# Kernel tuning notes

Measured on AMD Instinct MI355X. Metric: run time of the kernel, lower is better.

Reference implementation:

```python
import jax, jax.numpy as jnp
import numpy as np

HEAD_DIM = 32
NUM_HEADS = 8
NUM_ACTIONS = 16
IN_FEATURES = 512
HIDDEN = NUM_HEADS * HEAD_DIM
EPS = 1e-6


def _l2norm(v):
    return v / jnp.sqrt(jnp.sum(v * v, axis=-1, keepdims=True) + EPS)


def setup_inputs() -> dict:
    key = jax.random.key(0)
    ks = jax.random.split(key, 12)
    B, S = 4, 2048
    sc_x = 1.0 / np.sqrt(IN_FEATURES)
    sc_a = 1.0 / np.sqrt(NUM_ACTIONS)
    sc_h = 1.0 / np.sqrt(HIDDEN)
    return {
        "x": jax.random.normal(ks[0], (B, S, IN_FEATURES), jnp.float32),
        "action": jax.random.normal(ks[1], (B, S, NUM_ACTIONS), jnp.float32),
        "mask": jnp.zeros((B, S), jnp.float32),
        "carry": jnp.zeros((B, NUM_HEADS, HEAD_DIM, HEAD_DIM), jnp.float32),
        "Wq": jax.random.normal(ks[2], (IN_FEATURES, HIDDEN), jnp.float32) * sc_x,
        "Wk": jax.random.normal(ks[3], (IN_FEATURES, HIDDEN), jnp.float32) * sc_x,
        "Wv": jax.random.normal(ks[4], (IN_FEATURES, HIDDEN), jnp.float32) * sc_x,
        "Wbeta": jax.random.normal(ks[5], (IN_FEATURES, NUM_HEADS), jnp.float32) * sc_x,
        "Walpha": jax.random.normal(ks[6], (IN_FEATURES, NUM_HEADS), jnp.float32) * sc_x,
        "Wku": jax.random.normal(ks[7], (NUM_ACTIONS, HIDDEN), jnp.float32) * sc_a,
        "Wvu": jax.random.normal(ks[8], (NUM_ACTIONS, HIDDEN), jnp.float32) * sc_a,
        "Wgamma": jax.random.normal(ks[9], (NUM_ACTIONS, NUM_HEADS), jnp.float32) * sc_a,
        "rms_scale": jnp.ones((HIDDEN,), jnp.float32),
        "Wout": jax.random.normal(ks[10], (HIDDEN, IN_FEATURES), jnp.float32) * sc_h,
        "bout": jnp.zeros((IN_FEATURES,), jnp.float32),
    }


def reference(x, action, mask, carry, Wq, Wk, Wv, Wbeta, Walpha, Wku, Wvu,
              Wgamma, rms_scale, Wout, bout):
    B, S, F = x.shape
    H, D = NUM_HEADS, HEAD_DIM

    q_s = jax.nn.silu((x @ Wq).reshape(B, S, H, D))
    k_s = jax.nn.silu((x @ Wk).reshape(B, S, H, D))
    v_s = (x @ Wv).reshape(B, S, H, D)
    beta = jax.nn.sigmoid(x @ Wbeta)            # (B,S,H)
    A = jax.nn.sigmoid(x @ Walpha)              # (B,S,H)
    k_u = jax.nn.silu((action @ Wku).reshape(B, S, H, D))
    v_u = (action @ Wvu).reshape(B, S, H, D)
    Bg = jax.nn.sigmoid(action @ Wgamma)        # (B,S,H)

    q_s = _l2norm(q_s)
    k_s = _l2norm(k_s)
    k_u = _l2norm(k_u)

    eye = jnp.eye(D, dtype=x.dtype)
    kkT = jnp.einsum('bshi,bshj->bshij', k_s, k_s)
    delta = eye - beta[..., None, None] * kkT                      # (B,S,H,D,D)
    decay = A[..., None, None] * delta * (1.0 - mask[:, :, None, None, None])
    drift = Bg[..., None, None] * jnp.einsum('bshi,bshj->bshij', v_u, k_u)
    write = beta[..., None, None] * jnp.einsum('bshi,bshj->bshij', v_s, k_s)
    update = jnp.matmul(drift, delta) + write

    def binop(lhs, rhs):
        a_i, b_i = lhs
        a_j, b_j = rhs
        return (jnp.matmul(a_i, a_j), jnp.matmul(b_i, a_j) + b_j)

    cum_decay, hidden = jax.lax.associative_scan(binop, (decay, update), axis=1)
    hidden = jnp.matmul(carry[:, None], cum_decay) + hidden        # (B,S,H,D,D)

    out = jnp.einsum('bshij,bshj->bshi', hidden, q_s).reshape(B, S, H * D)
    out = out * jax.lax.rsqrt(jnp.mean(out * out, axis=-1, keepdims=True) + EPS)
    out = out * rms_scale
    y = out @ Wout + bout
    new_carry = hidden[:, -1]
    return (new_carry, y)
```

## Files before the change

kernel.cpp:

```cpp
#include <hip/hip_runtime.h>
#include <math.h>

constexpr int B_    = 4;
constexpr int S_    = 2048;
constexpr int F_    = 512;
constexpr int H_    = 8;
constexpr int D_    = 32;
constexpr int HID_  = 256;
constexpr int NA_   = 16;
constexpr int ROWS_ = B_ * S_;
constexpr int CHUNK_= 32;
constexpr int NC_   = S_ / CHUNK_;
constexpr int T_    = 16;
constexpr int NT_   = CHUNK_ / T_;
constexpr int BH_   = B_ * H_;

typedef __attribute__((ext_vector_type(8))) short short8;
typedef __attribute__((ext_vector_type(4))) float f32x4;
typedef unsigned short u16;

__device__ __forceinline__ float sigmoidf_(float x) { return 1.0f / (1.0f + expf(-x)); }

__device__ __forceinline__ u16 f2bf(float f) {
    unsigned u = __float_as_uint(f);
    return (u16)((u + 0x7FFF + ((u >> 16) & 1)) >> 16);
}
__device__ __forceinline__ float bf2f(u16 h) {
    return __uint_as_float(((unsigned)h) << 16);
}
__device__ __forceinline__ void bfsplit(float x, u16& hi, u16& lo) {
    hi = f2bf(x);
    lo = f2bf(x - bf2f(hi));
}

__device__ __forceinline__ unsigned swz(unsigned r, unsigned cbyte) {
    return cbyte ^ (((r >> 1) & 3) << 4);
}

__global__ __launch_bounds__(256) void conv_x_kernel(
    const float* __restrict__ x, u16* __restrict__ xh, u16* __restrict__ xl)
{
    const int idx = blockIdx.x * 256 + threadIdx.x;
    const float4 v = ((const float4*)x)[idx];
    ushort4 h, l;
    bfsplit(v.x, h.x, l.x); bfsplit(v.y, h.y, l.y);
    bfsplit(v.z, h.z, l.z); bfsplit(v.w, h.w, l.w);
    ((ushort4*)xh)[idx] = h;
    ((ushort4*)xl)[idx] = l;
}

__global__ __launch_bounds__(256) void conv_w_kernel(
    const float* __restrict__ Wq, const float* __restrict__ Wk,
    const float* __restrict__ Wv, const float* __restrict__ Wout,
    u16* __restrict__ wth, u16* __restrict__ wtl,
    u16* __restrict__ woth, u16* __restrict__ wotl)
{
    const int z = blockIdx.z;
    const float* src; u16 *dh, *dl; int R, C;
    if (z < 3) {
        src = (z == 0) ? Wq : (z == 1) ? Wk : Wv;
        R = 512; C = 256;
        dh = wth + (size_t)z * 256 * 512; dl = wtl + (size_t)z * 256 * 512;
    } else {
        src = Wout; R = 256; C = 512; dh = woth; dl = wotl;
    }
    const int r0 = blockIdx.x * 32, c0 = blockIdx.y * 32;
    if (r0 >= R || c0 >= C) return;
    __shared__ float tile[32][33];
    const int tx = threadIdx.x & 31, ty = threadIdx.x >> 5;
    #pragma unroll
    for (int i = 0; i < 4; i++)
        tile[ty + i * 8][tx] = src[(size_t)(r0 + ty + i * 8) * C + c0 + tx];
    __syncthreads();
    #pragma unroll
    for (int i = 0; i < 4; i++) {
        const float v = tile[tx][ty + i * 8];
        const size_t o = (size_t)(c0 + ty + i * 8) * R + r0 + tx;
        u16 h, l; bfsplit(v, h, l);
        dh[o] = h; dl[o] = l;
    }
}

__global__ __launch_bounds__(256) void conv_ba_kernel(
    const float* __restrict__ Wb, const float* __restrict__ Wa,
    u16* __restrict__ wbah, u16* __restrict__ wbal)
{
    const int idx = blockIdx.x * 256 + threadIdx.x;
    const int j = idx >> 9, k = idx & 511;
    const float v = (j < 8) ? Wb[(size_t)k * 8 + j] : Wa[(size_t)k * 8 + (j - 8)];
    u16 h, l; bfsplit(v, h, l);
    wbah[(size_t)j * 512 + k] = h;
    wbal[(size_t)j * 512 + k] = l;
}

__global__ __launch_bounds__(128) void mfma_gemm_kernel(
    const u16* __restrict__ Ah, const u16* __restrict__ Al,
    const u16* __restrict__ Bth, const u16* __restrict__ Btl,
    float* __restrict__ Cbase, int K, int N,
    int btStride, int cStride, const float* __restrict__ bias)
{
    const u16* bh_p = Bth + (size_t)blockIdx.z * btStride;
    const u16* bl_p = Btl + (size_t)blockIdx.z * btStride;
    float* C = Cbase + (size_t)blockIdx.z * cStride;

    __shared__ u16 lAh[128 * 32], lAl[128 * 32];
    __shared__ u16 lBh[64 * 32],  lBl[64 * 32];

    const int t    = threadIdx.x;
    const int wave = t >> 6;
    const int lane = t & 63;
    const int lr   = lane & 15;
    const int lk   = lane >> 4;
    const int row0 = blockIdx.x * 128;
    const int col0 = blockIdx.y * 64;

    f32x4 acc[4][4];
    #pragma unroll
    for (int i = 0; i < 4; i++)
        #pragma unroll
        for (int j = 0; j < 4; j++) acc[i][j] = (f32x4){0.f, 0.f, 0.f, 0.f};

    for (int k0 = 0; k0 < K; k0 += 32) {
        #pragma unroll
        for (int u = 0; u < 4; u++) {
            const int slot = t + u * 128;
            const int r = slot >> 2, cq = slot & 3;
            const size_t g = (size_t)(row0 + r) * K + k0 + cq * 8;
            const unsigned bo = r * 64 + swz(r, cq * 16);
            *(uint4*)((char*)lAh + bo) = *(const uint4*)(Ah + g);
            *(uint4*)((char*)lAl + bo) = *(const uint4*)(Al + g);
        }
        #pragma unroll
        for (int u = 0; u < 2; u++) {
            const int slot = t + u * 128;
            const int r = slot >> 2, cq = slot & 3;
            const size_t g = (size_t)(col0 + r) * K + k0 + cq * 8;
            const unsigned bo = r * 64 + swz(r, cq * 16);
            *(uint4*)((char*)lBh + bo) = *(const uint4*)(bh_p + g);
            *(uint4*)((char*)lBl + bo) = *(const uint4*)(bl_p + g);
        }
        __syncthreads();

        short8 ah[4], al[4];
        #pragma unroll
        for (int tm = 0; tm < 4; tm++) {
            const int r = wave * 64 + tm * 16 + lr;
            const unsigned bo = r * 64 + swz(r, lk * 16);
            ah[tm] = *(const short8*)((const char*)lAh + bo);
            al[tm] = *(const short8*)((const char*)lAl + bo);
        }
        #pragma unroll
        for (int tn = 0; tn < 4; tn++) {
            const int r = tn * 16 + lr;
            const unsigned bo = r * 64 + swz(r, lk * 16);
            const short8 bh = *(const short8*)((const char*)lBh + bo);
            const short8 bl = *(const short8*)((const char*)lBl + bo);
            #pragma unroll
            for (int tm = 0; tm < 4; tm++) {
                acc[tm][tn] = __builtin_amdgcn_mfma_f32_16x16x32_bf16(
                    ah[tm], bh, acc[tm][tn], 0, 0, 0);
                acc[tm][tn] = __builtin_amdgcn_mfma_f32_16x16x32_bf16(
                    ah[tm], bl, acc[tm][tn], 0, 0, 0);
                acc[tm][tn] = __builtin_amdgcn_mfma_f32_16x16x32_bf16(
                    al[tm], bh, acc[tm][tn], 0, 0, 0);
            }
        }
        __syncthreads();
    }

    #pragma unroll
    for (int tm = 0; tm < 4; tm++) {
        #pragma unroll
        for (int tn = 0; tn < 4; tn++) {
            const int col = col0 + tn * 16 + lr;
            const float b = bias ? bias[col] : 0.0f;
            #pragma unroll
            for (int v = 0; v < 4; v++) {
                const int row = row0 + wave * 64 + tm * 16 + lk * 4 + v;
                C[(size_t)row * N + col] = acc[tm][tn][v] + b;
            }
        }
    }
}

__global__ __launch_bounds__(256) void gemm_act_kernel(
    const float* __restrict__ act, const float* __restrict__ Wku,
    const float* __restrict__ Wvu, const float* __restrict__ Wg,
    float* __restrict__ ku, float* __restrict__ vu, float* __restrict__ bg)
{
    const int bid = blockIdx.x;
    if (bid < ROWS_ * 64 / 256) {
        const int idx = bid * 256 + threadIdx.x;
        const int row = idx >> 6, q = idx & 63, col = q * 4;
        float a[16];
        #pragma unroll
        for (int u = 0; u < 4; u++)
            *(float4*)&a[u*4] = *(const float4*)(act + (size_t)row * NA_ + u * 4);
        float4 accK = {0,0,0,0}, accV = {0,0,0,0};
        #pragma unroll
        for (int kk = 0; kk < NA_; kk++) {
            const float4 wk = *(const float4*)(Wku + (size_t)kk * HID_ + col);
            const float4 wv = *(const float4*)(Wvu + (size_t)kk * HID_ + col);
            accK.x += a[kk]*wk.x; accK.y += a[kk]*wk.y; accK.z += a[kk]*wk.z; accK.w += a[kk]*wk.w;
            accV.x += a[kk]*wv.x; accV.y += a[kk]*wv.y; accV.z += a[kk]*wv.z; accV.w += a[kk]*wv.w;
        }
        *(float4*)(ku + (size_t)row * HID_ + col) = accK;
        *(float4*)(vu + (size_t)row * HID_ + col) = accV;
    } else {
        const int idx = (bid - ROWS_ * 64 / 256) * 256 + threadIdx.x;
        const int row = idx >> 3, c = idx & 7;
        const float* a = act + (size_t)row * NA_;
        float acc = 0.0f;
        #pragma unroll
        for (int kk = 0; kk < NA_; kk++) acc += a[kk] * Wg[kk * H_ + c];
        bg[(size_t)row * H_ + c] = sigmoidf_(acc);
    }
}

__global__ __launch_bounds__(256) void silu_norm_kernel(
    float* __restrict__ q, float* __restrict__ k, float* __restrict__ ku)
{
    const int t = threadIdx.x;
    const int d = t & 31;
    const size_t g = (size_t)blockIdx.x * 8 + (t >> 5);
    const size_t idx = g * 32 + d;
    float* bufs[3] = { q, k, ku };
    #pragma unroll
    for (int a = 0; a < 3; a++) {
        float x = bufs[a][idx];
        float v = x * (1.0f / (1.0f + expf(-x)));
        float ss = v * v;
        ss += __shfl_xor(ss, 1);  ss += __shfl_xor(ss, 2);  ss += __shfl_xor(ss, 4);
        ss += __shfl_xor(ss, 8);  ss += __shfl_xor(ss, 16);
        bufs[a][idx] = v * rsqrtf(ss + 1e-6f);
    }
}

__global__ __launch_bounds__(256) void scan_pass1(
    const float* __restrict__ kbuf, const float* __restrict__ vbuf,
    const float* __restrict__ kubuf, const float* __restrict__ vubuf,
    const float* __restrict__ bab, const float* __restrict__ gammab,
    const float* __restrict__ mask,
    float* __restrict__ cumA, float* __restrict__ cumB)
{
    const int bh = blockIdx.x;
    const int c  = blockIdx.y;
    const int b  = bh >> 3, h = bh & 7;
    const int t  = threadIdx.x;
    const int i  = t >> 3;
    const int j0 = (t & 7) * 4;
    __shared__ float lk [T_][32];
    __shared__ float lv [T_][32];
    __shared__ float lku[T_][32];
    __shared__ float lvu[T_][32];
    __shared__ float lsc[T_][4];

    float M[4], Cc[4];
    #pragma unroll
    for (int jj = 0; jj < 4; jj++) { M[jj] = (i == j0 + jj) ? 1.0f : 0.0f; Cc[jj] = 0.0f; }

    const float* g0 = (t < 128) ? kbuf  : vbuf;
    const float* g1 = (t < 128) ? kubuf : vubuf;
    const int sr = (t >> 3) & 15, sq = t & 7;

    auto stage = [&](int tile, float4& n0, float4& n1, float& sc) {
        const int row_base = b * S_ + c * CHUNK_ + tile * T_;
        const size_t gb = (size_t)(row_base + sr) * HID_ + h * D_ + sq * 4;
        n0 = *(const float4*)(g0 + gb);
        n1 = *(const float4*)(g1 + gb);
        const int r = t & 15;
        const int rowi = row_base + r;
        if (t < 16)                     sc = sigmoidf_(bab[(size_t)rowi * 64 + h]);
        else if (t >= 64 && t < 80)     sc = sigmoidf_(bab[(size_t)rowi * 64 + 8 + h]) * (1.0f - mask[rowi]);
        else if (t >= 128 && t < 144)   sc = gammab[(size_t)rowi * H_ + h];
    };
    auto commit = [&](float4 n0, float4 n1, float sc) {
        if (t < 128) {
            *(float4*)&lk [sr][sq*4] = n0;
            *(float4*)&lku[sr][sq*4] = n1;
        } else {
            *(float4*)&lv [sr][sq*4] = n0;
            *(float4*)&lvu[sr][sq*4] = n1;
        }
        const int r = t & 15;
        if (t < 16)                     lsc[r][0] = sc;
        else if (t >= 64 && t < 80)     lsc[r][1] = sc;
        else if (t >= 128 && t < 144)   lsc[r][2] = sc;
    };

    float4 p0, p1; float psc = 0.0f;
    stage(0, p0, p1, psc);

    for (int tile = 0; tile < NT_; ++tile) {
        commit(p0, p1, psc);
        __syncthreads();
        float4 n0, n1; float nsc = 0.0f;
        if (tile + 1 < NT_) stage(tile + 1, n0, n1, nsc);

        #pragma unroll
        for (int sl = 0; sl < T_; sl++) {
            const float vi  = lv [sl][i];
            const float vui = lvu[sl][i];
            const float bet = lsc[sl][0];
            const float a   = lsc[sl][1];
            const float bgm = lsc[sl][2];
            float kj[4], kuj[4];
            *(float4*)kj  = *(const float4*)&lk [sl][j0];
            *(float4*)kuj = *(const float4*)&lku[sl][j0];
            float pd = 0.0f, mk = 0.0f, ck = 0.0f;
            #pragma unroll
            for (int jj = 0; jj < 4; jj++) {
                pd += kuj[jj] * kj[jj];
                mk += M[jj]   * kj[jj];
                ck += Cc[jj]  * kj[jj];
            }
            pd += __shfl_xor(pd, 1); pd += __shfl_xor(pd, 2); pd += __shfl_xor(pd, 4);
            mk += __shfl_xor(mk, 1); mk += __shfl_xor(mk, 2); mk += __shfl_xor(mk, 4);
            ck += __shfl_xor(ck, 1); ck += __shfl_xor(ck, 2); ck += __shfl_xor(ck, 4);
            const float abk_m   = a * bet * mk;
            const float ck_coef = bet * vi - a * bet * ck;
            const float wu      = bgm * vui;
            const float bduk    = bet * pd;
            #pragma unroll
            for (int jj = 0; jj < 4; jj++) {
                const float kv = kj[jj];
                const float w  = kuj[jj] - bduk * kv;
                M[jj]  = a * M[jj]  - abk_m   * kv;
                Cc[jj] = a * Cc[jj] + ck_coef * kv + wu * w;
            }
        }
        __syncthreads();
        p0 = n0; p1 = n1; psc = nsc;
    }
    const size_t ofs = ((size_t)(bh * NC_ + c)) * 1024 + (size_t)i * 32 + j0;
    *(float4*)(cumA + ofs) = make_float4(M[0],  M[1],  M[2],  M[3]);
    *(float4*)(cumB + ofs) = make_float4(Cc[0], Cc[1], Cc[2], Cc[3]);
}

__global__ __launch_bounds__(256) void scan_pass2(
    const float* __restrict__ carry, const float* __restrict__ cumA,
    const float* __restrict__ cumB, float* __restrict__ Sstart,
    float* __restrict__ carry_out)
{
    const int bh = blockIdx.x;
    const int t  = threadIdx.x;
    const int i  = t >> 3;
    const int j0 = (t & 7) * 4;
    __shared__ float Ash[2][32][36];
    __shared__ float Ssh[2][32][36];

    const size_t idx  = (size_t)i * 32 + j0;
    const size_t base = (size_t)bh * NC_ * 1024;

    float4 Sv = *(const float4*)(carry + (size_t)bh * 1024 + idx);
    float4 Areg = *(const float4*)(cumA + base + idx);
    float4 Breg = *(const float4*)(cumB + base + idx);

    *(float4*)&Ssh[0][i][j0] = Sv;
    *(float4*)&Ash[0][i][j0] = Areg;
    __syncthreads();

    int buf = 0;
    for (int c = 0; c < NC_; c++) {
        *(float4*)(Sstart + base + (size_t)c * 1024 + idx) = Sv;
        float4 Areg2, Breg2;
        if (c + 1 < NC_) {
            Areg2 = *(const float4*)(cumA + base + (size_t)(c + 1) * 1024 + idx);
            Breg2 = *(const float4*)(cumB + base + (size_t)(c + 1) * 1024 + idx);
        }
        float s[32];
        #pragma unroll
        for (int g = 0; g < 8; g++)
            *(float4*)&s[g*4] = *(const float4*)&Ssh[buf][i][g*4];
        float4 acc = Breg;
        #pragma unroll
        for (int m = 0; m < 32; m++) {
            const float4 a4 = *(const float4*)&Ash[buf][m][j0];
            acc.x += s[m] * a4.x; acc.y += s[m] * a4.y;
            acc.z += s[m] * a4.z; acc.w += s[m] * a4.w;
        }
        Sv = acc;
        if (c + 1 < NC_) {
            *(float4*)&Ash[buf ^ 1][i][j0] = Areg2;
            *(float4*)&Ssh[buf ^ 1][i][j0] = Sv;
            Areg = Areg2; Breg = Breg2;
        }
        __syncthreads();
        buf ^= 1;
    }
    *(float4*)(carry_out + (size_t)bh * 1024 + idx) = Sv;
}

__global__ __launch_bounds__(256) void scan_pass3(
    const float* __restrict__ qbuf, const float* __restrict__ kbuf,
    const float* __restrict__ vbuf, const float* __restrict__ kubuf,
    const float* __restrict__ vubuf, const float* __restrict__ bab,
    const float* __restrict__ gammab, const float* __restrict__ mask,
    const float* __restrict__ Sstart, float* __restrict__ outpre)
{
    const int bh = blockIdx.x, c = blockIdx.y;
    const int b  = bh >> 3, h = bh & 7;
    const int t  = threadIdx.x;
    const int i  = t >> 3;
    const int j0 = (t & 7) * 4;
    __shared__ float lk [T_][32];
    __shared__ float lq [T_][32];
    __shared__ float lv [T_][32];
    __shared__ float lku[T_][32];
    __shared__ float lvu[T_][32];
    __shared__ float lsc[T_][4];

    float Sv[4];
    const size_t sofs = ((size_t)(bh * NC_ + c)) * 1024 + (size_t)i * 32 + j0;
    {
        float4 s4 = *(const float4*)(Sstart + sofs);
        Sv[0] = s4.x; Sv[1] = s4.y; Sv[2] = s4.z; Sv[3] = s4.w;
    }

    const float* g0 = (t < 128) ? kbuf  : vbuf;
    const float* g1 = (t < 128) ? kubuf : vubuf;
    const int sr = (t >> 3) & 15, sq = t & 7;

    auto stage = [&](int tile, float4& n0, float4& n1, float4& n2, float& sc) {
        const int row_base = b * S_ + c * CHUNK_ + tile * T_;
        const size_t gb = (size_t)(row_base + sr) * HID_ + h * D_ + sq * 4;
        n0 = *(const float4*)(g0 + gb);
        n1 = *(const float4*)(g1 + gb);
        if (t < 128) n2 = *(const float4*)(qbuf + gb);
        const int r = t & 15;
        const int rowi = row_base + r;
        if (t < 16)                     sc = sigmoidf_(bab[(size_t)rowi * 64 + h]);
        else if (t >= 64 && t < 80)     sc = sigmoidf_(bab[(size_t)rowi * 64 + 8 + h]) * (1.0f - mask[rowi]);
        else if (t >= 128 && t < 144)   sc = gammab[(size_t)rowi * H_ + h];
    };
    auto commit = [&](float4 n0, float4 n1, float4 n2, float sc) {
        if (t < 128) {
            *(float4*)&lk [sr][sq*4] = n0;
            *(float4*)&lku[sr][sq*4] = n1;
            *(float4*)&lq [sr][sq*4] = n2;
        } else {
            *(float4*)&lv [sr][sq*4] = n0;
            *(float4*)&lvu[sr][sq*4] = n1;
        }
        const int r = t & 15;
        if (t < 16)                     lsc[r][0] = sc;
        else if (t >= 64 && t < 80)     lsc[r][1] = sc;
        else if (t >= 128 && t < 144)   lsc[r][2] = sc;
    };

    float4 p0, p1, p2; float psc = 0.0f;
    stage(0, p0, p1, p2, psc);

    for (int tile = 0; tile < NT_; ++tile) {
        commit(p0, p1, p2, psc);
        __syncthreads();
        float4 n0, n1, n2; float nsc = 0.0f;
        if (tile + 1 < NT_) stage(tile + 1, n0, n1, n2, nsc);

        const int row_base = b * S_ + c * CHUNK_ + tile * T_;
        #pragma unroll
        for (int sl = 0; sl < T_; sl++) {
            const float vi  = lv [sl][i];
            const float vui = lvu[sl][i];
            const float bet = lsc[sl][0];
            const float a   = lsc[sl][1];
            const float bgm = lsc[sl][2];
            float kj[4], kuj[4], qj[4];
            *(float4*)kj  = *(const float4*)&lk [sl][j0];
            *(float4*)kuj = *(const float4*)&lku[sl][j0];
            *(float4*)qj  = *(const float4*)&lq [sl][j0];
            float pd = 0.0f, sk = 0.0f;
            #pragma unroll
            for (int jj = 0; jj < 4; jj++) {
                pd += kuj[jj] * kj[jj];
                sk += Sv[jj]  * kj[jj];
            }
            pd += __shfl_xor(pd, 1); pd += __shfl_xor(pd, 2); pd += __shfl_xor(pd, 4);
            sk += __shfl_xor(sk, 1); sk += __shfl_xor(sk, 2); sk += __shfl_xor(sk, 4);
            const float coef_k = bet * vi - a * bet * sk;
            const float wu     = bgm * vui;
            const float bduk   = bet * pd;
            float op = 0.0f;
            #pragma unroll
            for (int jj = 0; jj < 4; jj++) {
                const float kv = kj[jj];
                const float w  = kuj[jj] - bduk * kv;
                Sv[jj] = a * Sv[jj] + coef_k * kv + wu * w;
                op += Sv[jj] * qj[jj];
            }
            op += __shfl_xor(op, 1); op += __shfl_xor(op, 2); op += __shfl_xor(op, 4);
            if ((t & 7) == 0)
                outpre[(size_t)(row_base + sl) * HID_ + h * D_ + i] = op;
        }
        __syncthreads();
        p0 = n0; p1 = n1; p2 = n2; psc = nsc;
    }
}

__global__ __launch_bounds__(256) void rms_conv_kernel(
    const float* __restrict__ outpre, const float* __restrict__ rms_scale,
    u16* __restrict__ onh, u16* __restrict__ onl)
{
    const int t = threadIdx.x;
    const int lane = t & 63;
    const int row = blockIdx.x * 4 + (t >> 6);
    const float4 v = ((const float4*)(outpre + (size_t)row * HID_))[lane];
    float ss = v.x*v.x + v.y*v.y + v.z*v.z + v.w*v.w;
    ss += __shfl_xor(ss, 1);  ss += __shfl_xor(ss, 2);  ss += __shfl_xor(ss, 4);
    ss += __shfl_xor(ss, 8);  ss += __shfl_xor(ss, 16); ss += __shfl_xor(ss, 32);
    const float rinv = rsqrtf(ss * (1.0f / HID_) + 1e-6f);
    const float4 sc = ((const float4*)rms_scale)[lane];
    ushort4 h, l;
    bfsplit(v.x * rinv * sc.x, h.x, l.x);
    bfsplit(v.y * rinv * sc.y, h.y, l.y);
    bfsplit(v.z * rinv * sc.z, h.z, l.z);
    bfsplit(v.w * rinv * sc.w, h.w, l.w);
    ((ushort4*)(onh + (size_t)row * HID_))[lane] = h;
    ((ushort4*)(onl + (size_t)row * HID_))[lane] = l;
}

extern "C" void kernel_launch(void* const* d_in, const int* in_sizes, int n_in,
                              void* d_out, int out_size, void* d_ws, size_t ws_size,
                              hipStream_t stream)
{
    const float* x      = (const float*)d_in[0];
    const float* action = (const float*)d_in[1];
    const float* mask   = (const float*)d_in[2];
    const float* carry  = (const float*)d_in[3];
    const float* Wq     = (const float*)d_in[4];
    const float* Wk     = (const float*)d_in[5];
    const float* Wv     = (const float*)d_in[6];
    const float* Wbeta  = (const float*)d_in[7];
    const float* Walpha = (const float*)d_in[8];
    const float* Wku    = (const float*)d_in[9];
    const float* Wvu    = (const float*)d_in[10];
    const float* Wgamma = (const float*)d_in[11];
    const float* rms_s  = (const float*)d_in[12];
    const float* Wout   = (const float*)d_in[13];
    const float* bout   = (const float*)d_in[14];

    float* carry_out = (float*)d_out;
    float* y         = (float*)d_out + (size_t)BH_ * D_ * D_;

    float* ws = (float*)d_ws;
    float* qb     = ws; ws += (size_t)ROWS_ * HID_;
    float* kb     = ws; ws += (size_t)ROWS_ * HID_;
    float* vb     = ws; ws += (size_t)ROWS_ * HID_;
    float* kub    = ws; ws += (size_t)ROWS_ * HID_;
    float* vub    = ws; ws += (size_t)ROWS_ * HID_;
    float* bab    = ws; ws += (size_t)ROWS_ * 64;
    float* gammab = ws; ws += (size_t)ROWS_ * H_;
    float* cumA   = ws; ws += (size_t)BH_ * NC_ * D_ * D_;
    float* cumB   = ws; ws += (size_t)BH_ * NC_ * D_ * D_;
    u16* xh       = (u16*)ws;
    float* outpre = ws; ws += (size_t)ROWS_ * HID_;
    u16* xl       = (u16*)ws; ws += (size_t)ROWS_ * F_ / 2;
    u16* wth      = (u16*)ws; ws += (size_t)3 * HID_ * F_ / 2;
    u16* wtl      = (u16*)ws; ws += (size_t)3 * HID_ * F_ / 2;
    u16* woth     = (u16*)ws; ws += (size_t)F_ * HID_ / 2;
    u16* wotl     = (u16*)ws; ws += (size_t)F_ * HID_ / 2;
    u16* wbah     = (u16*)ws; ws += (size_t)64 * F_ / 2;
    u16* wbal     = (u16*)ws; ws += (size_t)64 * F_ / 2;
    float* Sst    = cumA;
    u16* onh = (u16*)qb;
    u16* onl = (u16*)qb + (size_t)ROWS_ * HID_;

    conv_x_kernel<<<dim3(ROWS_ * F_ / 4 / 256), 256, 0, stream>>>(x, xh, xl);
    conv_w_kernel<<<dim3(16, 16, 4), 256, 0, stream>>>(
        Wq, Wk, Wv, Wout, wth, wtl, woth, wotl);
    conv_ba_kernel<<<dim3(16 * F_ / 256), 256, 0, stream>>>(Wbeta, Walpha, wbah, wbal);
    mfma_gemm_kernel<<<dim3(ROWS_/128, HID_/64, 3), 128, 0, stream>>>(
        xh, xl, wth, wtl, qb, F_, HID_, HID_ * F_, ROWS_ * HID_, nullptr);
    mfma_gemm_kernel<<<dim3(ROWS_/128, 1, 1), 128, 0, stream>>>(
        xh, xl, wbah, wbal, bab, F_, 64, 0, 0, nullptr);
    gemm_act_kernel<<<dim3(ROWS_ * 64 / 256 + ROWS_ * 8 / 256), 256, 0, stream>>>(
        action, Wku, Wvu, Wgamma, kub, vub, gammab);
    silu_norm_kernel<<<dim3(ROWS_*H_/8), 256, 0, stream>>>(qb, kb, kub);
    scan_pass1<<<dim3(BH_, NC_), 256, 0, stream>>>(
        kb, vb, kub, vub, bab, gammab, mask, cumA, cumB);
    scan_pass2<<<dim3(BH_), 256, 0, stream>>>(carry, cumA, cumB, Sst, carry_out);
    scan_pass3<<<dim3(BH_, NC_), 256, 0, stream>>>(
        qb, kb, vb, kub, vub, bab, gammab, mask, Sst, outpre);
    rms_conv_kernel<<<dim3(ROWS_/4), 256, 0, stream>>>(outpre, rms_s, onh, onl);
    mfma_gemm_kernel<<<dim3(ROWS_/128, F_/64, 1), 128, 0, stream>>>(
        onh, onl, woth, wotl, y, HID_, F_, 0, 0, bout);
}
```

Baseline: 309.4 us.

## Fuse scan passes 1 and 3 via per-step query projections and matmul assembly

Replaces the two sequential per-chunk scan passes (state summary, then re-scan with the true start state) with one intra-chunk scan. Alongside the cumulative matrices, it emits per-step vectors z (query projected through the cumulative decay) and y (local output). A new kernel then rebuilds outputs as Sstart·z + y, a small dense contraction per chunk. Per-token dot products (k·ku, k·q, ku·q) are precomputed in the silu/norm kernel to shorten the recurrence's dependency chain. This removes a full sequential scan pass, at the cost of extra z/y buffer traffic and more reductions per step inside the fused scan.

Result: faster. 290.9 us (-6.0%).

```diff
diff --git a/kernel.cpp b/kernel.cpp
--- a/kernel.cpp
+++ b/kernel.cpp
@@ -218,187 +218,48 @@
 }
 
 __global__ __launch_bounds__(256) void silu_norm_kernel(
-    float* __restrict__ q, float* __restrict__ k, float* __restrict__ ku)
+    float* __restrict__ q, float* __restrict__ k, float* __restrict__ ku,
+    float* __restrict__ dukb, float* __restrict__ kqb, float* __restrict__ kuqb)
 {
     const int t = threadIdx.x;
     const int d = t & 31;
     const size_t g = (size_t)blockIdx.x * 8 + (t >> 5);
     const size_t idx = g * 32 + d;
-    float* bufs[3] = { q, k, ku };
-    #pragma unroll
-    for (int a = 0; a < 3; a++) {
-        float x = bufs[a][idx];
-        float v = x * (1.0f / (1.0f + expf(-x)));
-        float ss = v * v;
-        ss += __shfl_xor(ss, 1);  ss += __shfl_xor(ss, 2);  ss += __shfl_xor(ss, 4);
-        ss += __shfl_xor(ss, 8);  ss += __shfl_xor(ss, 16);
-        bufs[a][idx] = v * rsqrtf(ss + 1e-6f);
-    }
-}
-
-__global__ __launch_bounds__(256) void scan_pass1(
-    const float* __restrict__ kbuf, const float* __restrict__ vbuf,
-    const float* __restrict__ kubuf, const float* __restrict__ vubuf,
-    const float* __restrict__ bab, const float* __restrict__ gammab,
-    const float* __restrict__ mask,
-    float* __restrict__ cumA, float* __restrict__ cumB)
-{
-    const int bh = blockIdx.x;
-    const int c  = blockIdx.y;
-    const int b  = bh >> 3, h = bh & 7;
-    const int t  = threadIdx.x;
-    const int i  = t >> 3;
-    const int j0 = (t & 7) * 4;
-    __shared__ float lk [T_][32];
-    __shared__ float lv [T_][32];
-    __shared__ float lku[T_][32];
-    __shared__ float lvu[T_][32];
-    __shared__ float lsc[T_][4];
-
-    float M[4], Cc[4];
-    #pragma unroll
-    for (int jj = 0; jj < 4; jj++) { M[jj] = (i == j0 + jj) ? 1.0f : 0.0f; Cc[jj] = 0.0f; }
-
-    const float* g0 = (t < 128) ? kbuf  : vbuf;
-    const float* g1 = (t < 128) ? kubuf : vubuf;
-    const int sr = (t >> 3) & 15, sq = t & 7;
-
-    auto stage = [&](int tile, float4& n0, float4& n1, float& sc) {
-        const int row_base = b * S_ + c * CHUNK_ + tile * T_;
-        const size_t gb = (size_t)(row_base + sr) * HID_ + h * D_ + sq * 4;
-        n0 = *(const float4*)(g0 + gb);
-        n1 = *(const float4*)(g1 + gb);
-        const int r = t & 15;
-        const int rowi = row_base + r;
-        if (t < 16)                     sc = sigmoidf_(bab[(size_t)rowi * 64 + h]);
-        else if (t >= 64 && t < 80)     sc = sigmoidf_(bab[(size_t)rowi * 64 + 8 + h]) * (1.0f - mask[rowi]);
-        else if (t >= 128 && t < 144)   sc = gammab[(size_t)rowi * H_ + h];
-    };
-    auto commit = [&](float4 n0, float4 n1, float sc) {
-        if (t < 128) {
-            *(float4*)&lk [sr][sq*4] = n0;
-            *(float4*)&lku[sr][sq*4] = n1;
-        } else {
-            *(float4*)&lv [sr][sq*4] = n0;
-            *(float4*)&lvu[sr][sq*4] = n1;
-        }
-        const int r = t & 15;
-        if (t < 16)                     lsc[r][0] = sc;
-        else if (t >= 64 && t < 80)     lsc[r][1] = sc;
-        else if (t >= 128 && t < 144)   lsc[r][2] = sc;
-    };
-
-    float4 p0, p1; float psc = 0.0f;
-    stage(0, p0, p1, psc);
-
-    for (int tile = 0; tile < NT_; ++tile) {
-        commit(p0, p1, psc);
-        __syncthreads();
-        float4 n0, n1; float nsc = 0.0f;
-        if (tile + 1 < NT_) stage(tile + 1, n0, n1, nsc);
-
-        #pragma unroll
-        for (int sl = 0; sl < T_; sl++) {
-            const float vi  = lv [sl][i];
-            const float vui = lvu[sl][i];
-            const float bet = lsc[sl][0];
-            const float a   = lsc[sl][1];
-            const float bgm = lsc[sl][2];
-            float kj[4], kuj[4];
-            *(float4*)kj  = *(const float4*)&lk [sl][j0];
-            *(float4*)kuj = *(const float4*)&lku[sl][j0];
-            float pd = 0.0f, mk = 0.0f, ck = 0.0f;
-            #pragma unroll
-            for (int jj = 0; jj < 4; jj++) {
-                pd += kuj[jj] * kj[jj];
-                mk += M[jj]   * kj[jj];
-                ck += Cc[jj]  * kj[jj];
-            }
-            pd += __shfl_xor(pd, 1); pd += __shfl_xor(pd, 2); pd += __shfl_xor(pd, 4);
-            mk += __shfl_xor(mk, 1); mk += __shfl_xor(mk, 2); mk += __shfl_xor(mk, 4);
-            ck += __shfl_xor(ck, 1); ck += __shfl_xor(ck, 2); ck += __shfl_xor(ck, 4);
-            const float abk_m   = a * bet * mk;
-            const float ck_coef = bet * vi - a * bet * ck;
-            const float wu      = bgm * vui;
-            const float bduk    = bet * pd;
-            #pragma unroll
-            for (int jj = 0; jj < 4; jj++) {
-                const float kv = kj[jj];
-                const float w  = kuj[jj] - bduk * kv;
-                M[jj]  = a * M[jj]  - abk_m   * kv;
-                Cc[jj] = a * Cc[jj] + ck_coef * kv + wu * w;
-            }
-        }
-        __syncthreads();
-        p0 = n0; p1 = n1; psc = nsc;
-    }
-    const size_t ofs = ((size_t)(bh * NC_ + c)) * 1024 + (size_t)i * 32 + j0;
-    *(float4*)(cumA + ofs) = make_float4(M[0],  M[1],  M[2],  M[3]);
-    *(float4*)(cumB + ofs) = make_float4(Cc[0], Cc[1], Cc[2], Cc[3]);
-}
-
-__global__ __launch_bounds__(256) void scan_pass2(
-    const float* __restrict__ carry, const float* __restrict__ cumA,
-    const float* __restrict__ cumB, float* __restrict__ Sstart,
-    float* __restrict__ carry_out)
-{
-    const int bh = blockIdx.x;
-    const int t  = threadIdx.x;
-    const int i  = t >> 3;
-    const int j0 = (t & 7) * 4;
-    __shared__ float Ash[2][32][36];
-    __shared__ float Ssh[2][32][36];
-
-    const size_t idx  = (size_t)i * 32 + j0;
-    const size_t base = (size_t)bh * NC_ * 1024;
-
-    float4 Sv = *(const float4*)(carry + (size_t)bh * 1024 + idx);
-    float4 Areg = *(const float4*)(cumA + base + idx);
-    float4 Breg = *(const float4*)(cumB + base + idx);
-
-    *(float4*)&Ssh[0][i][j0] = Sv;
-    *(float4*)&Ash[0][i][j0] = Areg;
-    __syncthreads();
-
-    int buf = 0;
-    for (int c = 0; c < NC_; c++) {
-        *(float4*)(Sstart + base + (size_t)c * 1024 + idx) = Sv;
-        float4 Areg2, Breg2;
-        if (c + 1 < NC_) {
-            Areg2 = *(const float4*)(cumA + base + (size_t)(c + 1) * 1024 + idx);
-            Breg2 = *(const float4*)(cumB + base + (size_t)(c + 1) * 1024 + idx);
-        }
-        float s[32];
-        #pragma unroll
-        for (int g = 0; g < 8; g++)
-            *(float4*)&s[g*4] = *(const float4*)&Ssh[buf][i][g*4];
-        float4 acc = Breg;
-        #pragma unroll
-        for (int m = 0; m < 32; m++) {
-            const float4 a4 = *(const float4*)&Ash[buf][m][j0];
-            acc.x += s[m] * a4.x; acc.y += s[m] * a4.y;
-            acc.z += s[m] * a4.z; acc.w += s[m] * a4.w;
-        }
-        Sv = acc;
-        if (c + 1 < NC_) {
-            *(float4*)&Ash[buf ^ 1][i][j0] = Areg2;
-            *(float4*)&Ssh[buf ^ 1][i][j0] = Sv;
-            Areg = Areg2; Breg = Breg2;
-        }
-        __syncthreads();
-        buf ^= 1;
-    }
-    *(float4*)(carry_out + (size_t)bh * 1024 + idx) = Sv;
-}
-
-__global__ __launch_bounds__(256) void scan_pass3(
+    const float xq = q[idx], xk = k[idx], xku = ku[idx];
+    const float vq = xq * (1.0f / (1.0f + expf(-xq)));
+    const float vk = xk * (1.0f / (1.0f + expf(-xk)));
+    const float vu = xku * (1.0f / (1.0f + expf(-xku)));
+    float sq = vq * vq, sk = vk * vk, su = vu * vu;
+    #pragma unroll
+    for (int m = 1; m < 32; m <<= 1) {
+        sq += __shfl_xor(sq, m); sk += __shfl_xor(sk, m); su += __shfl_xor(su, m);
+    }
+    const float nq = vq * rsqrtf(sq + 1e-6f);
+    const float nk = vk * rsqrtf(sk + 1e-6f);
+    const float nu = vu * rsqrtf(su + 1e-6f);
+    q[idx] = nq; k[idx] = nk; ku[idx] = nu;
+    float duk = nk * nu, kq = nk * nq, kuq = nu * nq;
+    #pragma unroll
+    for (int m = 1; m < 32; m <<= 1) {
+        duk += __shfl_xor(duk, m); kq += __shfl_xor(kq, m); kuq += __shfl_xor(kuq, m);
+    }
+    if (d == 0)      dukb[g] = duk;
+    else if (d == 1) kqb[g]  = kq;
+    else if (d == 2) kuqb[g] = kuq;
+}
+
+__global__ __launch_bounds__(256) void scan_fused(
     const float* __restrict__ qbuf, const float* __restrict__ kbuf,
     const float* __restrict__ vbuf, const float* __restrict__ kubuf,
     const float* __restrict__ vubuf, const float* __restrict__ bab,
-    const float* __restrict__ gammab, const float* __restrict__ mask,
-    const float* __restrict__ Sstart, float* __restrict__ outpre)
-{
-    const int bh = blockIdx.x, c = blockIdx.y;
+    const float* __restrict__ gammab, const float* __restrict__ dukb,
+    const float* __restrict__ kqb, const float* __restrict__ kuqb,
+    const float* __restrict__ mask,
+    float* __restrict__ cumA, float* __restrict__ cumB,
+    float* __restrict__ zbuf, float* __restrict__ ybuf)
+{
+    const int bh = blockIdx.x;
+    const int c  = blockIdx.y;
     const int b  = bh >> 3, h = bh & 7;
     const int t  = threadIdx.x;
     const int i  = t >> 3;
@@ -408,14 +269,11 @@
     __shared__ float lv [T_][32];
     __shared__ float lku[T_][32];
     __shared__ float lvu[T_][32];
-    __shared__ float lsc[T_][4];
-
-    float Sv[4];
-    const size_t sofs = ((size_t)(bh * NC_ + c)) * 1024 + (size_t)i * 32 + j0;
-    {
-        float4 s4 = *(const float4*)(Sstart + sofs);
-        Sv[0] = s4.x; Sv[1] = s4.y; Sv[2] = s4.z; Sv[3] = s4.w;
-    }
+    __shared__ float lsc[T_][8];
+
+    float M[4], Cc[4];
+    #pragma unroll
+    for (int jj = 0; jj < 4; jj++) { M[jj] = (i == j0 + jj) ? 1.0f : 0.0f; Cc[jj] = 0.0f; }
 
     const float* g0 = (t < 128) ? kbuf  : vbuf;
     const float* g1 = (t < 128) ? kubuf : vubuf;
@@ -430,8 +288,11 @@
         const int r = t & 15;
         const int rowi = row_base + r;
         if (t < 16)                     sc = sigmoidf_(bab[(size_t)rowi * 64 + h]);
+        else if (t < 32)                sc = dukb[(size_t)rowi * H_ + h];
         else if (t >= 64 && t < 80)     sc = sigmoidf_(bab[(size_t)rowi * 64 + 8 + h]) * (1.0f - mask[rowi]);
+        else if (t >= 80 && t < 96)     sc = kqb[(size_t)rowi * H_ + h];
         else if (t >= 128 && t < 144)   sc = gammab[(size_t)rowi * H_ + h];
+        else if (t >= 144 && t < 160)   sc = kuqb[(size_t)rowi * H_ + h];
     };
     auto commit = [&](float4 n0, float4 n1, float4 n2, float sc) {
         if (t < 128) {
@@ -444,8 +305,11 @@
         }
         const int r = t & 15;
         if (t < 16)                     lsc[r][0] = sc;
+        else if (t < 32)                lsc[r][3] = sc;
         else if (t >= 64 && t < 80)     lsc[r][1] = sc;
+        else if (t >= 80 && t < 96)     lsc[r][4] = sc;
         else if (t >= 128 && t < 144)   lsc[r][2] = sc;
+        else if (t >= 144 && t < 160)   lsc[r][5] = sc;
     };
 
     float4 p0, p1, p2; float psc = 0.0f;
@@ -457,7 +321,6 @@
         float4 n0, n1, n2; float nsc = 0.0f;
         if (tile + 1 < NT_) stage(tile + 1, n0, n1, n2, nsc);
 
-        const int row_base = b * S_ + c * CHUNK_ + tile * T_;
         #pragma unroll
         for (int sl = 0; sl < T_; sl++) {
             const float vi  = lv [sl][i];
@@ -465,36 +328,138 @@
             const float bet = lsc[sl][0];
             const float a   = lsc[sl][1];
             const float bgm = lsc[sl][2];
+            const float duk = lsc[sl][3];
+            const float kq  = lsc[sl][4];
+            const float kuq = lsc[sl][5];
             float kj[4], kuj[4], qj[4];
             *(float4*)kj  = *(const float4*)&lk [sl][j0];
             *(float4*)kuj = *(const float4*)&lku[sl][j0];
             *(float4*)qj  = *(const float4*)&lq [sl][j0];
-            float pd = 0.0f, sk = 0.0f;
+            const float bduk = bet * duk;
+            const float bkq  = bet * kq;
+            float uj[4];
+            #pragma unroll
+            for (int jj = 0; jj < 4; jj++) uj[jj] = qj[jj] - bkq * kj[jj];
+            float mk = 0.0f, ck = 0.0f, zq = 0.0f, cq = 0.0f;
             #pragma unroll
             for (int jj = 0; jj < 4; jj++) {
-                pd += kuj[jj] * kj[jj];
-                sk += Sv[jj]  * kj[jj];
+                mk += M[jj]  * kj[jj];
+                ck += Cc[jj] * kj[jj];
+                zq += M[jj]  * uj[jj];
+                cq += Cc[jj] * uj[jj];
             }
-            pd += __shfl_xor(pd, 1); pd += __shfl_xor(pd, 2); pd += __shfl_xor(pd, 4);
-            sk += __shfl_xor(sk, 1); sk += __shfl_xor(sk, 2); sk += __shfl_xor(sk, 4);
-            const float coef_k = bet * vi - a * bet * sk;
-            const float wu     = bgm * vui;
-            const float bduk   = bet * pd;
-            float op = 0.0f;
+            mk += __shfl_xor(mk, 1); ck += __shfl_xor(ck, 1);
+            zq += __shfl_xor(zq, 1); cq += __shfl_xor(cq, 1);
+            mk += __shfl_xor(mk, 2); ck += __shfl_xor(ck, 2);
+            zq += __shfl_xor(zq, 2); cq += __shfl_xor(cq, 2);
+            mk += __shfl_xor(mk, 4); ck += __shfl_xor(ck, 4);
+            zq += __shfl_xor(zq, 4); cq += __shfl_xor(cq, 4);
+            const float am    = a * bet * mk;
+            const float wu    = bgm * vui;
+            const float kcoef = bet * vi - a * bet * ck - wu * bduk;
+            const float zt    = a * zq;
+            const float yt    = a * cq + wu * (kuq - bduk * kq) + bet * kq * vi;
             #pragma unroll
             for (int jj = 0; jj < 4; jj++) {
-                const float kv = kj[jj];
-                const float w  = kuj[jj] - bduk * kv;
-                Sv[jj] = a * Sv[jj] + coef_k * kv + wu * w;
-                op += Sv[jj] * qj[jj];
+                M[jj]  = a * M[jj]  - am * kj[jj];
+                Cc[jj] = a * Cc[jj] + kcoef * kj[jj] + wu * kuj[jj];
             }
-            op += __shfl_xor(op, 1); op += __shfl_xor(op, 2); op += __shfl_xor(op, 4);
-            if ((t & 7) == 0)
-                outpre[(size_t)(row_base + sl) * HID_ + h * D_ + i] = op;
+            const size_t zofs = (((size_t)(bh * NC_ + c)) * CHUNK_ + tile * T_ + sl) * 32;
+            if ((t & 7) == 0)      zbuf[zofs + i] = zt;
+            else if ((t & 7) == 1) ybuf[zofs + i] = yt;
         }
         __syncthreads();
         p0 = n0; p1 = n1; p2 = n2; psc = nsc;
     }
+    const size_t ofs = ((size_t)(bh * NC_ + c)) * 1024 + (size_t)i * 32 + j0;
+    *(float4*)(cumA + ofs) = make_float4(M[0],  M[1],  M[2],  M[3]);
+    *(float4*)(cumB + ofs) = make_float4(Cc[0], Cc[1], Cc[2], Cc[3]);
+}
+
+__global__ __launch_bounds__(256) void scan_pass2(
+    const float* __restrict__ carry, const float* __restrict__ cumA,
+    const float* __restrict__ cumB, float* __restrict__ Sstart,
+    float* __restrict__ carry_out)
+{
+    const int bh = blockIdx.x;
+    const int t  = threadIdx.x;
+    const int i  = t >> 3;
+    const int j0 = (t & 7) * 4;
+    __shared__ float Ash[2][32][36];
+    __shared__ float Ssh[2][32][36];
+
+    const size_t idx  = (size_t)i * 32 + j0;
+    const size_t base = (size_t)bh * NC_ * 1024;
+
+    float4 Sv = *(const float4*)(carry + (size_t)bh * 1024 + idx);
+    float4 Areg = *(const float4*)(cumA + base + idx);
+    float4 Breg = *(const float4*)(cumB + base + idx);
+
+    *(float4*)&Ssh[0][i][j0] = Sv;
+    *(float4*)&Ash[0][i][j0] = Areg;
+    __syncthreads();
+
+    int buf = 0;
+    for (int c = 0; c < NC_; c++) {
+        *(float4*)(Sstart + base + (size_t)c * 1024 + idx) = Sv;
+        float4 Areg2, Breg2;
+        if (c + 1 < NC_) {
+            Areg2 = *(const float4*)(cumA + base + (size_t)(c + 1) * 1024 + idx);
+            Breg2 = *(const float4*)(cumB + base + (size_t)(c + 1) * 1024 + idx);
+        }
+        float s[32];
+        #pragma unroll
+        for (int g = 0; g < 8; g++)
+            *(float4*)&s[g*4] = *(const float4*)&Ssh[buf][i][g*4];
+        float4 acc = Breg;
+        #pragma unroll
+        for (int m = 0; m < 32; m++) {
+            const float4 a4 = *(const float4*)&Ash[buf][m][j0];
+            acc.x += s[m] * a4.x; acc.y += s[m] * a4.y;
+            acc.z += s[m] * a4.z; acc.w += s[m] * a4.w;
+        }
+        Sv = acc;
+        if (c + 1 < NC_) {
+            *(float4*)&Ash[buf ^ 1][i][j0] = Areg2;
+            *(float4*)&Ssh[buf ^ 1][i][j0] = Sv;
+            Areg = Areg2; Breg = Breg2;
+        }
+        __syncthreads();
+        buf ^= 1;
+    }
+    *(float4*)(carry_out + (size_t)bh * 1024 + idx) = Sv;
+}
+
+__global__ __launch_bounds__(256) void out_asm_kernel(
+    const float* __restrict__ Sstart, const float* __restrict__ zbuf,
+    const float* __restrict__ ybuf, float* __restrict__ outpre)
+{
+    const int bh = blockIdx.x, c = blockIdx.y;
+    const int b  = bh >> 3, h = bh & 7;
+    const int t  = threadIdx.x;
+    __shared__ float Ssh[32][33];
+    __shared__ float Zsh[32][33];
+    const size_t ofs = ((size_t)(bh * NC_ + c)) * 1024;
+    {
+        const float4 s4 = *(const float4*)(Sstart + ofs + t * 4);
+        *(float4*)&Ssh[t >> 3][(t & 7) * 4] = s4;
+        const float4 z4 = *(const float4*)(zbuf + ofs + t * 4);
+        *(float4*)&Zsh[t >> 3][(t & 7) * 4] = z4;
+    }
+    __syncthreads();
+    const int tt = t >> 3;
+    const int iq = (t & 7) * 4;
+    float4 acc = *(const float4*)(ybuf + ofs + (size_t)tt * 32 + iq);
+    #pragma unroll
+    for (int j = 0; j < 32; j++) {
+        const float zj = Zsh[tt][j];
+        acc.x += Ssh[iq + 0][j] * zj;
+        acc.y += Ssh[iq + 1][j] * zj;
+        acc.z += Ssh[iq + 2][j] * zj;
+        acc.w += Ssh[iq + 3][j] * zj;
+    }
+    const int s = c * CHUNK_ + tt;
+    *(float4*)(outpre + ((size_t)(b * S_ + s)) * HID_ + h * D_ + iq) = acc;
 }
 
 __global__ __launch_bounds__(256) void rms_conv_kernel(
@@ -550,8 +515,13 @@
     float* vub    = ws; ws += (size_t)ROWS_ * HID_;
     float* bab    = ws; ws += (size_t)ROWS_ * 64;
     float* gammab = ws; ws += (size_t)ROWS_ * H_;
+    float* dukb   = ws; ws += (size_t)ROWS_ * H_;
+    float* kqb    = ws; ws += (size_t)ROWS_ * H_;
+    float* kuqb   = ws; ws += (size_t)ROWS_ * H_;
     float* cumA   = ws; ws += (size_t)BH_ * NC_ * D_ * D_;
     float* cumB   = ws; ws += (size_t)BH_ * NC_ * D_ * D_;
+    float* zbuf   = ws; ws += (size_t)BH_ * S_ * D_;
+    float* ybuf   = ws; ws += (size_t)BH_ * S_ * D_;
     u16* xh       = (u16*)ws;
     float* outpre = ws; ws += (size_t)ROWS_ * HID_;
     u16* xl       = (u16*)ws; ws += (size_t)ROWS_ * F_ / 2;
@@ -575,12 +545,13 @@
         xh, xl, wbah, wbal, bab, F_, 64, 0, 0, nullptr);
     gemm_act_kernel<<<dim3(ROWS_ * 64 / 256 + ROWS_ * 8 / 256), 256, 0, stream>>>(
         action, Wku, Wvu, Wgamma, kub, vub, gammab);
-    silu_norm_kernel<<<dim3(ROWS_*H_/8), 256, 0, stream>>>(qb, kb, kub);
-    scan_pass1<<<dim3(BH_, NC_), 256, 0, stream>>>(
-        kb, vb, kub, vub, bab, gammab, mask, cumA, cumB);
+    silu_norm_kernel<<<dim3(ROWS_*H_/8), 256, 0, stream>>>(
+        qb, kb, kub, dukb, kqb, kuqb);
+    scan_fused<<<dim3(BH_, NC_), 256, 0, stream>>>(
+        qb, kb, vb, kub, vub, bab, gammab, dukb, kqb, kuqb, mask,
+        cumA, cumB, zbuf, ybuf);
     scan_pass2<<<dim3(BH_), 256, 0, stream>>>(carry, cumA, cumB, Sst, carry_out);
-    scan_pass3<<<dim3(BH_, NC_), 256, 0, stream>>>(
-        qb, kb, vb, kub, vub, bab, gammab, mask, Sst, outpre);
+    out_asm_kernel<<<dim3(BH_, NC_), 256, 0, stream>>>(Sst, zbuf, ybuf, outpre);
     rms_conv_kernel<<<dim3(ROWS_/4), 256, 0, stream>>>(outpre, rms_s, onh, onl);
     mfma_gemm_kernel<<<dim3(ROWS_/128, F_/64, 1), 128, 0, stream>>>(
         onh, onl, woth, wotl, y, HID_, F_, 0, 0, bout);
```
